# Performance work log

Measured on AMD Instinct MI355X. Metric: run time of the kernel, lower is better.

The kernel has to match this reference:

```python
import jax, jax.numpy as jnp
import numpy as np

IN_DIM = 3
OUT_DIM = 3
HIDDEN = [40, 40, 40, 40, 40, 40]
N_POINTS = 2_097_152


def _glorot(key, fan_in, fan_out):
    std = jnp.sqrt(2.0 / (fan_in + fan_out)).astype(jnp.float32)
    return jax.random.normal(key, (fan_in, fan_out), dtype=jnp.float32) * std


def setup_inputs() -> dict:
    key = jax.random.key(0)
    keys = jax.random.split(key, 8)
    coords = jax.random.uniform(keys[0], (N_POINTS, IN_DIM), dtype=jnp.float32)
    dims = [IN_DIM] + HIDDEN + [OUT_DIM]  # [3,40,40,40,40,40,40,3]
    inp = {"coords": coords}
    for i in range(7):
        inp[f"W{i}"] = _glorot(keys[i + 1], dims[i], dims[i + 1])
        inp[f"b{i}"] = jnp.zeros((dims[i + 1],), dtype=jnp.float32)
    return inp


def reference(coords, W0, b0, W1, b1, W2, b2, W3, b3, W4, b4, W5, b5, W6, b6):
    # 7-layer coordinate MLP: Linear+Tanh x6, final Linear. coords: [N,3] -> [N,3]
    Ws = [W0, W1, W2, W3, W4, W5, W6]
    bs = [b0, b1, b2, b3, b4, b5, b6]
    x = coords
    for i in range(6):
        x = jnp.tanh(x @ Ws[i] + bs[i])
    return x @ Ws[6] + bs[6]
```

## Files before the change

### kernel.cpp

```cpp
#include <hip/hip_runtime.h>


typedef _Float16 f16x8 __attribute__((ext_vector_type(8)));
typedef float    f32x16 __attribute__((ext_vector_type(16)));
typedef unsigned int u32x4 __attribute__((ext_vector_type(4)));

#define NFRAG  35
#define TABN   225
#define TABREP 32
#define SEXP   6
#define INVH   32.0f
#define UOFF   112.0f
#define UMAX   223.999f
#define TABR   3.5f
#define EXPSC  2.8853900817779268f

__constant__ int INV[48] = {
     0,  1,  2,  3,   8,  9, 10, 11,   4,  5,  6,  7,  12, 13, 14, 15,
    16, 17, 18, 19,  24, 25, 26, 27,  20, 21, 22, 23,  28, 29, 30, 31,
    32, 33, 34, 35,  -1, -1, -1, -1,  36, 37, 38, 39,  -2, -3, -1, -1 };

__constant__ int KAP[40] = {
     0,  1,  2,  3,   8,  9, 10, 11,   4,  5,  6,  7,  12, 13, 14, 15,
    16, 17, 18, 19,  24, 25, 26, 27,  20, 21, 22, 23,  28, 29, 30, 31,
    32, 33, 34, 35,  40, 41, 42, 43 };

__global__ void prep_frags(const float* __restrict__ W0, const float* __restrict__ b0,
                           const float* __restrict__ W1, const float* __restrict__ b1,
                           const float* __restrict__ W2, const float* __restrict__ b2,
                           const float* __restrict__ W3, const float* __restrict__ b3,
                           const float* __restrict__ W4, const float* __restrict__ b4,
                           const float* __restrict__ W5, const float* __restrict__ b5,
                           const float* __restrict__ W6, const float* __restrict__ b6,
                           unsigned short* __restrict__ frags,
                           unsigned* __restrict__ table)
{
    int tid = blockIdx.x * 256 + threadIdx.x;

    if (tid < NFRAG * 64) {
        int frag = tid >> 6, lane = tid & 63;

        int layer, mt, ch;
        if (frag < 2)       { layer = 0; mt = frag; ch = 0; }
        else if (frag < 32) { int t = frag - 2; layer = 1 + t / 6; int r = t % 6; mt = r / 3; ch = r % 3; }
        else                { layer = 6; mt = 0; ch = frag - 32; }

        const float* Ws[7] = { W0, W1, W2, W3, W4, W5, W6 };
        const float* bs[7] = { b0, b1, b2, b3, b4, b5, b6 };
        const float* W = Ws[layer];
        const float* b = bs[layer];
        const int fout = (layer == 6) ? 3 : 40;

        int jout  = mt * 32 + (lane & 31);
        int kbase = ch * 16 + (lane >> 5) * 8;

        unsigned short h[8];
        for (int i = 0; i < 8; ++i) {
            int k = kbase + i;
            float v = 0.0f;
            if (jout < fout) {
                int jin;
                if (layer == 0) jin = (k < 3) ? k : ((k == 3) ? -2 : ((k == 4) ? -3 : -1));
                else            jin = INV[k];
                bool ex = false;
                if (layer < 6) {
                    int kp = KAP[jout];
                    int P = 4 * (kp >> 4) + ((kp & 7) >> 1);
                    ex = (P < SEXP);
                }
                float scale = (layer == 6) ? 1.0f : (ex ? EXPSC : INVH);
                if (jin >= 0)       v = W[jin * fout + jout] * scale;
                else if (jin == -2) v = b[jout] * scale;
                else if (jin == -3) v = (layer == 6 || ex) ? 0.0f : UOFF;
            }
            _Float16 hv = (_Float16)v;
            h[i] = __builtin_bit_cast(unsigned short, hv);
        }
        unsigned short* dst = frags + frag * 512 + lane * 8;
        for (int i = 0; i < 8; ++i) dst[i] = h[i];
    }
    else if (tid < NFRAG * 64 + TABN) {
        int i = tid - NFRAG * 64;
        const float H = 1.0f / 32.0f;
        float x  = -TABR + (float)i * H;
        float t0 = tanhf(x);
        float t1 = tanhf(x + H);
        float MID = 0.5f * (1.0f + tanhf(TABR));
        float base = t0, delta = t1 - t0;
        if (i == 0)        { base = -MID; delta = t1 - base; }
        if (i == TABN - 2) { delta = MID - t0; }
        unsigned short bb = __builtin_bit_cast(unsigned short, (_Float16)base);
        unsigned short dd = __builtin_bit_cast(unsigned short, (_Float16)delta);
        table[i] = (unsigned)bb | ((unsigned)dd << 16);
    }
}

__device__ __forceinline__ unsigned int pkf16(float a, float b) {
    return __builtin_bit_cast(unsigned int, __builtin_amdgcn_cvt_pkrtz(a, b));
}
__device__ __forceinline__ f32x16 zf() {
    f32x16 v;
    #pragma unroll
    for (int i = 0; i < 16; ++i) v[i] = 0.0f;
    return v;
}
__device__ __forceinline__ float exp2_fast(float y) {
#if __has_builtin(__builtin_amdgcn_exp2f)
    return __builtin_amdgcn_exp2f(y);
#else
    float e;
    asm("v_exp_f32 %0, %1" : "=v"(e) : "v"(y));
    return e;
#endif
}

#define MFMA __builtin_amdgcn_mfma_f32_32x32x16_f16

#define ACT(Da, Db, Bfx) do {                         \
    Bfx[0]  = pkf16(te(Da[0]),  te(Da[1]));           \
    Bfx[1]  = pkf16(te(Da[2]),  te(Da[3]));           \
    Bfx[2]  = pkf16(te(Da[4]),  te(Da[5]));           \
    Bfx[3]  = pkf16(te(Da[6]),  te(Da[7]));           \
    Bfx[4]  = pkf16(te(Da[8]),  te(Da[9]));           \
    Bfx[5]  = pkf16(te(Da[10]), te(Da[11]));          \
    Bfx[6]  = tl2(Da[12], Da[13]);                    \
    Bfx[7]  = tl2(Da[14], Da[15]);                    \
    Bfx[8]  = tl2(Db[0],  Db[1]);                     \
    Bfx[9]  = tl2(Db[2],  Db[3]);                     \
    Bfx[10] = PK11;                                   \
    Bfx[11] = 0u;                                     \
} while (0)

__global__ __launch_bounds__(512, 4) void mlp_mfma(const float* __restrict__ coords,
                                                   const unsigned short* __restrict__ frags,
                                                   const unsigned* __restrict__ gtab,
                                                   float* __restrict__ out, int npts)
{
    __shared__ __align__(16) unsigned short sf[NFRAG * 512];
    __shared__ __align__(16) unsigned stab[TABN * TABREP];
    {
        const u32x4* s1 = (const u32x4*)frags; u32x4* d1 = (u32x4*)sf;
        for (int i = threadIdx.x; i < NFRAG * 64; i += 512) d1[i] = s1[i];
        for (int i = threadIdx.x; i < TABN * TABREP; i += 512) stab[i] = gtab[i >> 5];
    }
    __syncthreads();

    const int lane = threadIdx.x & 63;
    const int wid  = threadIdx.x >> 6;
    const int pA   = (blockIdx.x * 8 + wid) * 64 + (lane & 31);
    const int pB   = pA + 32;
    const bool vA = (pA < npts), vB = (pB < npts);

    float cA0 = 0.f, cA1 = 0.f, cA2 = 0.f, cB0 = 0.f, cB1 = 0.f, cB2 = 0.f;
    if (vA) { cA0 = coords[pA * 3]; cA1 = coords[pA * 3 + 1]; cA2 = coords[pA * 3 + 2]; }
    if (vB) { cB0 = coords[pB * 3]; cB1 = coords[pB * 3 + 1]; cB2 = coords[pB * 3 + 2]; }

    const unsigned int PK11 = pkf16(1.0f, 1.0f);
    const unsigned* __restrict__ tb = stab + (lane & 31);
    const f32x16 CZ = zf();

    auto tl2 = [&](float ua, float ub) -> unsigned {
        ua = __builtin_amdgcn_fmed3f(ua, 0.0f, UMAX);
        ub = __builtin_amdgcn_fmed3f(ub, 0.0f, UMAX);
        float fa = __builtin_amdgcn_fractf(ua);
        float fb = __builtin_amdgcn_fractf(ub);
        unsigned ea = tb[(unsigned)ua * TABREP];
        unsigned eb = tb[(unsigned)ub * TABREP];
        unsigned r;
        asm("v_fma_mixlo_f16 %0, %1, %2, %2 op_sel:[0,1,0] op_sel_hi:[0,1,1]"
            : "=v"(r) : "v"(fa), "v"(ea));
        asm("v_fma_mixhi_f16 %0, %1, %2, %2 op_sel:[0,1,0] op_sel_hi:[0,1,1]"
            : "+v"(r) : "v"(fb), "v"(eb));
        return r;
    };
    auto te = [&](float y) -> float {
        float e = exp2_fast(y);
        float r = __builtin_amdgcn_rcpf(e + 1.0f);
        return __builtin_fmaf(-2.0f, r, 1.0f);
    };

    unsigned int BfA[12], BfB[12];
    BfA[0] = pkf16(cA0, cA1); BfA[1] = pkf16(cA2, 1.0f);
    BfA[2] = pkf16(1.0f, 0.0f); BfA[3] = 0u;
    BfB[0] = pkf16(cB0, cB1); BfB[1] = pkf16(cB2, 1.0f);
    BfB[2] = pkf16(1.0f, 0.0f); BfB[3] = 0u;

    auto AF = [&](int f) -> f16x8 {
        return ((const f16x8*)sf)[f * 64 + lane];
    };
    auto BFx = [&](const unsigned (&B)[12], int c) -> f16x8 {
        u32x4 t = { B[4 * c + 0], B[4 * c + 1], B[4 * c + 2], B[4 * c + 3] };
        return __builtin_bit_cast(f16x8, t);
    };

    f16x8 F0, F1, F2, F3, F4, F5;

    F0 = AF(0); F1 = AF(1);
    {
        f32x16 D0 = MFMA(F0, BFx(BfA, 0), CZ, 0, 0, 0);
        f32x16 D1 = MFMA(F1, BFx(BfA, 0), CZ, 0, 0, 0);
        ACT(D0, D1, BfA);
    }
    {
        f32x16 D0 = MFMA(F0, BFx(BfB, 0), CZ, 0, 0, 0);
        f32x16 D1 = MFMA(F1, BFx(BfB, 0), CZ, 0, 0, 0);
        ACT(D0, D1, BfB);
    }

    #pragma unroll
    for (int l = 1; l <= 5; ++l) {
        const int fb = 2 + (l - 1) * 6;
        F0 = AF(fb + 0); F1 = AF(fb + 1); F2 = AF(fb + 2);
        F3 = AF(fb + 3); F4 = AF(fb + 4); F5 = AF(fb + 5);
        {
            f16x8 B0 = BFx(BfA, 0), B1 = BFx(BfA, 1), B2 = BFx(BfA, 2);
            f32x16 D0 = MFMA(F0, B0, CZ, 0, 0, 0);
            D0 = MFMA(F1, B1, D0, 0, 0, 0);
            D0 = MFMA(F2, B2, D0, 0, 0, 0);
            f32x16 D1 = MFMA(F3, B0, CZ, 0, 0, 0);
            D1 = MFMA(F4, B1, D1, 0, 0, 0);
            D1 = MFMA(F5, B2, D1, 0, 0, 0);
            ACT(D0, D1, BfA);
        }
        {
            f16x8 B0 = BFx(BfB, 0), B1 = BFx(BfB, 1), B2 = BFx(BfB, 2);
            f32x16 D0 = MFMA(F0, B0, CZ, 0, 0, 0);
            D0 = MFMA(F1, B1, D0, 0, 0, 0);
            D0 = MFMA(F2, B2, D0, 0, 0, 0);
            f32x16 D1 = MFMA(F3, B0, CZ, 0, 0, 0);
            D1 = MFMA(F4, B1, D1, 0, 0, 0);
            D1 = MFMA(F5, B2, D1, 0, 0, 0);
            ACT(D0, D1, BfB);
        }
    }

    F0 = AF(32); F1 = AF(33); F2 = AF(34);
    {
        f32x16 D0 = MFMA(F0, BFx(BfA, 0), CZ, 0, 0, 0);
        D0 = MFMA(F1, BFx(BfA, 1), D0, 0, 0, 0);
        D0 = MFMA(F2, BFx(BfA, 2), D0, 0, 0, 0);
        if (lane < 32 && vA) {
            out[pA * 3 + 0] = D0[0];
            out[pA * 3 + 1] = D0[1];
            out[pA * 3 + 2] = D0[2];
        }
    }
    {
        f32x16 D0 = MFMA(F0, BFx(BfB, 0), CZ, 0, 0, 0);
        D0 = MFMA(F1, BFx(BfB, 1), D0, 0, 0, 0);
        D0 = MFMA(F2, BFx(BfB, 2), D0, 0, 0, 0);
        if (lane < 32 && vB) {
            out[pB * 3 + 0] = D0[0];
            out[pB * 3 + 1] = D0[1];
            out[pB * 3 + 2] = D0[2];
        }
    }
}

extern "C" void kernel_launch(void* const* d_in, const int* in_sizes, int n_in,
                              void* d_out, int out_size, void* d_ws, size_t ws_size,
                              hipStream_t stream)
{
    const float* coords = (const float*)d_in[0];
    const float* W0 = (const float*)d_in[1];  const float* b0 = (const float*)d_in[2];
    const float* W1 = (const float*)d_in[3];  const float* b1 = (const float*)d_in[4];
    const float* W2 = (const float*)d_in[5];  const float* b2 = (const float*)d_in[6];
    const float* W3 = (const float*)d_in[7];  const float* b3 = (const float*)d_in[8];
    const float* W4 = (const float*)d_in[9];  const float* b4 = (const float*)d_in[10];
    const float* W5 = (const float*)d_in[11]; const float* b5 = (const float*)d_in[12];
    const float* W6 = (const float*)d_in[13]; const float* b6 = (const float*)d_in[14];
    float* out = (float*)d_out;

    unsigned short* frags = (unsigned short*)d_ws;
    unsigned* table = (unsigned*)((char*)d_ws + NFRAG * 1024);

    const int npts = in_sizes[0] / 3;

    const int prep_threads = NFRAG * 64 + TABN;
    prep_frags<<<(prep_threads + 255) / 256, 256, 0, stream>>>(
        W0, b0, W1, b1, W2, b2, W3, b3, W4, b4, W5, b5, W6, b6, frags, table);

    const int blocks = (npts + 511) / 512;
    mlp_mfma<<<blocks, 512, 0, stream>>>(coords, frags, table, out, npts);
}
```

Before: 111.9 us.

## Process four 32-point tiles per wave and shift more tanh work to table lookup

Each wave now handles 128 points in four 32-column tiles instead of 64 points in two, and the grid is halved to match. Weight fragments loaded from LDS are reused across more MFMAs, and there are more independent MFMA chains available to hide latency. The activation split also changes: six fewer outputs per tile use exp/rcp tanh and six more use the shared-memory interpolation table, with SEXP reduced from 6 to 3 accordingly. This raises register pressure and possibly LDS bank traffic from table lookups, and may alter accuracy.

```diff
diff --git a/kernel.cpp b/kernel.cpp
--- a/kernel.cpp
+++ b/kernel.cpp
@@ -8,7 +8,7 @@
 #define NFRAG  35
 #define TABN   225
 #define TABREP 32
-#define SEXP   6
+#define SEXP   3
 #define INVH   32.0f
 #define UOFF   112.0f
 #define UMAX   223.999f
@@ -120,15 +120,44 @@
     Bfx[0]  = pkf16(te(Da[0]),  te(Da[1]));           \
     Bfx[1]  = pkf16(te(Da[2]),  te(Da[3]));           \
     Bfx[2]  = pkf16(te(Da[4]),  te(Da[5]));           \
-    Bfx[3]  = pkf16(te(Da[6]),  te(Da[7]));           \
-    Bfx[4]  = pkf16(te(Da[8]),  te(Da[9]));           \
-    Bfx[5]  = pkf16(te(Da[10]), te(Da[11]));          \
+    Bfx[3]  = tl2(Da[6],  Da[7]);                     \
+    Bfx[4]  = tl2(Da[8],  Da[9]);                     \
+    Bfx[5]  = tl2(Da[10], Da[11]);                    \
     Bfx[6]  = tl2(Da[12], Da[13]);                    \
     Bfx[7]  = tl2(Da[14], Da[15]);                    \
     Bfx[8]  = tl2(Db[0],  Db[1]);                     \
     Bfx[9]  = tl2(Db[2],  Db[3]);                     \
     Bfx[10] = PK11;                                   \
     Bfx[11] = 0u;                                     \
+} while (0)
+
+#define L0_TILE(Bfx) do {                             \
+    f16x8 bb = BFx(Bfx, 0);                           \
+    f32x16 D0 = MFMA(F0, bb, CZ, 0, 0, 0);            \
+    f32x16 D1 = MFMA(F1, bb, CZ, 0, 0, 0);            \
+    ACT(D0, D1, Bfx);                                 \
+} while (0)
+
+#define HID_TILE(Bfx) do {                            \
+    f16x8 B0 = BFx(Bfx, 0), B1 = BFx(Bfx, 1), B2 = BFx(Bfx, 2); \
+    f32x16 D0 = MFMA(F0, B0, CZ, 0, 0, 0);            \
+    D0 = MFMA(F1, B1, D0, 0, 0, 0);                   \
+    D0 = MFMA(F2, B2, D0, 0, 0, 0);                   \
+    f32x16 D1 = MFMA(F3, B0, CZ, 0, 0, 0);            \
+    D1 = MFMA(F4, B1, D1, 0, 0, 0);                   \
+    D1 = MFMA(F5, B2, D1, 0, 0, 0);                   \
+    ACT(D0, D1, Bfx);                                 \
+} while (0)
+
+#define FIN_TILE(Bfx, pX, vX) do {                    \
+    f32x16 D0 = MFMA(F0, BFx(Bfx, 0), CZ, 0, 0, 0);   \
+    D0 = MFMA(F1, BFx(Bfx, 1), D0, 0, 0, 0);          \
+    D0 = MFMA(F2, BFx(Bfx, 2), D0, 0, 0, 0);          \
+    if (lane < 32 && vX) {                            \
+        out[(pX) * 3 + 0] = D0[0];                    \
+        out[(pX) * 3 + 1] = D0[1];                    \
+        out[(pX) * 3 + 2] = D0[2];                    \
+    }                                                 \
 } while (0)
 
 __global__ __launch_bounds__(512, 4) void mlp_mfma(const float* __restrict__ coords,
@@ -147,13 +176,11 @@
 
     const int lane = threadIdx.x & 63;
     const int wid  = threadIdx.x >> 6;
-    const int pA   = (blockIdx.x * 8 + wid) * 64 + (lane & 31);
+    const int pA   = (blockIdx.x * 8 + wid) * 128 + (lane & 31);
     const int pB   = pA + 32;
-    const bool vA = (pA < npts), vB = (pB < npts);
-
-    float cA0 = 0.f, cA1 = 0.f, cA2 = 0.f, cB0 = 0.f, cB1 = 0.f, cB2 = 0.f;
-    if (vA) { cA0 = coords[pA * 3]; cA1 = coords[pA * 3 + 1]; cA2 = coords[pA * 3 + 2]; }
-    if (vB) { cB0 = coords[pB * 3]; cB1 = coords[pB * 3 + 1]; cB2 = coords[pB * 3 + 2]; }
+    const int pC   = pA + 64;
+    const int pD   = pA + 96;
+    const bool vA = (pA < npts), vB = (pB < npts), vC = (pC < npts), vD = (pD < npts);
 
     const unsigned int PK11 = pkf16(1.0f, 1.0f);
     const unsigned* __restrict__ tb = stab + (lane & 31);
@@ -179,11 +206,21 @@
         return __builtin_fmaf(-2.0f, r, 1.0f);
     };
 
-    unsigned int BfA[12], BfB[12];
-    BfA[0] = pkf16(cA0, cA1); BfA[1] = pkf16(cA2, 1.0f);
-    BfA[2] = pkf16(1.0f, 0.0f); BfA[3] = 0u;
-    BfB[0] = pkf16(cB0, cB1); BfB[1] = pkf16(cB2, 1.0f);
-    BfB[2] = pkf16(1.0f, 0.0f); BfB[3] = 0u;
+    unsigned int BfA[12], BfB[12], BfC[12], BfD[12];
+    {
+        float a0 = 0.f, a1 = 0.f, a2 = 0.f, b0 = 0.f, b1 = 0.f, b2 = 0.f;
+        float c0 = 0.f, c1 = 0.f, c2 = 0.f, d0 = 0.f, d1 = 0.f, d2 = 0.f;
+        if (vA) { a0 = coords[pA * 3]; a1 = coords[pA * 3 + 1]; a2 = coords[pA * 3 + 2]; }
+        if (vB) { b0 = coords[pB * 3]; b1 = coords[pB * 3 + 1]; b2 = coords[pB * 3 + 2]; }
+        if (vC) { c0 = coords[pC * 3]; c1 = coords[pC * 3 + 1]; c2 = coords[pC * 3 + 2]; }
+        if (vD) { d0 = coords[pD * 3]; d1 = coords[pD * 3 + 1]; d2 = coords[pD * 3 + 2]; }
+        BfA[0] = pkf16(a0, a1); BfA[1] = pkf16(a2, 1.0f);
+        BfB[0] = pkf16(b0, b1); BfB[1] = pkf16(b2, 1.0f);
+        BfC[0] = pkf16(c0, c1); BfC[1] = pkf16(c2, 1.0f);
+        BfD[0] = pkf16(d0, d1); BfD[1] = pkf16(d2, 1.0f);
+        BfA[2] = BfB[2] = BfC[2] = BfD[2] = pkf16(1.0f, 0.0f);
+        BfA[3] = BfB[3] = BfC[3] = BfD[3] = 0u;
+    }
 
     auto AF = [&](int f) -> f16x8 {
         return ((const f16x8*)sf)[f * 64 + lane];
@@ -196,65 +233,21 @@
     f16x8 F0, F1, F2, F3, F4, F5;
 
     F0 = AF(0); F1 = AF(1);
-    {
-        f32x16 D0 = MFMA(F0, BFx(BfA, 0), CZ, 0, 0, 0);
-        f32x16 D1 = MFMA(F1, BFx(BfA, 0), CZ, 0, 0, 0);
-        ACT(D0, D1, BfA);
-    }
-    {
-        f32x16 D0 = MFMA(F0, BFx(BfB, 0), CZ, 0, 0, 0);
-        f32x16 D1 = MFMA(F1, BFx(BfB, 0), CZ, 0, 0, 0);
-        ACT(D0, D1, BfB);
-    }
+    L0_TILE(BfA); L0_TILE(BfB); L0_TILE(BfC); L0_TILE(BfD);
 
     #pragma unroll
     for (int l = 1; l <= 5; ++l) {
         const int fb = 2 + (l - 1) * 6;
         F0 = AF(fb + 0); F1 = AF(fb + 1); F2 = AF(fb + 2);
         F3 = AF(fb + 3); F4 = AF(fb + 4); F5 = AF(fb + 5);
-        {
-            f16x8 B0 = BFx(BfA, 0), B1 = BFx(BfA, 1), B2 = BFx(BfA, 2);
-            f32x16 D0 = MFMA(F0, B0, CZ, 0, 0, 0);
-            D0 = MFMA(F1, B1, D0, 0, 0, 0);
-            D0 = MFMA(F2, B2, D0, 0, 0, 0);
-            f32x16 D1 = MFMA(F3, B0, CZ, 0, 0, 0);
-            D1 = MFMA(F4, B1, D1, 0, 0, 0);
-            D1 = MFMA(F5, B2, D1, 0, 0, 0);
-            ACT(D0, D1, BfA);
-        }
-        {
-            f16x8 B0 = BFx(BfB, 0), B1 = BFx(BfB, 1), B2 = BFx(BfB, 2);
-            f32x16 D0 = MFMA(F0, B0, CZ, 0, 0, 0);
-            D0 = MFMA(F1, B1, D0, 0, 0, 0);
-            D0 = MFMA(F2, B2, D0, 0, 0, 0);
-            f32x16 D1 = MFMA(F3, B0, CZ, 0, 0, 0);
-            D1 = MFMA(F4, B1, D1, 0, 0, 0);
-            D1 = MFMA(F5, B2, D1, 0, 0, 0);
-            ACT(D0, D1, BfB);
-        }
+        HID_TILE(BfA); HID_TILE(BfB); HID_TILE(BfC); HID_TILE(BfD);
     }
 
     F0 = AF(32); F1 = AF(33); F2 = AF(34);
-    {
-        f32x16 D0 = MFMA(F0, BFx(BfA, 0), CZ, 0, 0, 0);
-        D0 = MFMA(F1, BFx(BfA, 1), D0, 0, 0, 0);
-        D0 = MFMA(F2, BFx(BfA, 2), D0, 0, 0, 0);
-        if (lane < 32 && vA) {
-            out[pA * 3 + 0] = D0[0];
-            out[pA * 3 + 1] = D0[1];
-            out[pA * 3 + 2] = D0[2];
-        }
-    }
-    {
-        f32x16 D0 = MFMA(F0, BFx(BfB, 0), CZ, 0, 0, 0);
-        D0 = MFMA(F1, BFx(BfB, 1), D0, 0, 0, 0);
-        D0 = MFMA(F2, BFx(BfB, 2), D0, 0, 0, 0);
-        if (lane < 32 && vB) {
-            out[pB * 3 + 0] = D0[0];
-            out[pB * 3 + 1] = D0[1];
-            out[pB * 3 + 2] = D0[2];
-        }
-    }
+    FIN_TILE(BfA, pA, vA);
+    FIN_TILE(BfB, pB, vB);
+    FIN_TILE(BfC, pC, vC);
+    FIN_TILE(BfD, pD, vD);
 }
 
 extern "C" void kernel_launch(void* const* d_in, const int* in_sizes, int n_in,
@@ -280,6 +273,6 @@
     prep_frags<<<(prep_threads + 255) / 256, 256, 0, stream>>>(
         W0, b0, W1, b1, W2, b2, W3, b3, W4, b4, W5, b5, W6, b6, frags, table);
 
-    const int blocks = (npts + 511) / 512;
+    const int blocks = (npts + 1023) / 1024;
     mlp_mfma<<<blocks, 512, 0, stream>>>(coords, frags, table, out, npts);
 }
```

New measurement: 121.2 us. 8.3% more time.
